# Performance work log

Hardware: AMD Instinct MI355X
Metric: run time of the kernel (lower is better)

## Reference

```python
import jax, jax.numpy as jnp
import numpy as np
from jax import lax

B, S, V, E, H, T = 128, 512, 30000, 256, 256, 9
PAD_ID = 0


def setup_inputs() -> dict:
    key = jax.random.key(0)
    ks = jax.random.split(key, 16)
    u = lambda k, sh, s: jax.random.uniform(k, sh, jnp.float32, -s, s)
    sc = 1.0 / float(np.sqrt(H))
    so = 1.0 / float(np.sqrt(2 * H))
    input_ids = jax.random.randint(ks[0], (B, S), 1, V)
    lengths = jax.random.randint(ks[1], (B,), 1, S + 1)
    mask = jnp.arange(S)[None, :] < lengths[:, None]  # left-contiguous valid mask
    embed_table = jax.random.normal(ks[2], (V, E), jnp.float32).at[PAD_ID].set(0.0)
    return dict(
        input_ids=input_ids,
        mask=mask,
        embed_table=embed_table,
        W_ih_f=u(ks[3], (4 * H, E), sc), W_hh_f=u(ks[4], (4 * H, H), sc), b_f=u(ks[5], (4 * H,), sc),
        W_ih_b=u(ks[6], (4 * H, E), sc), W_hh_b=u(ks[7], (4 * H, H), sc), b_b=u(ks[8], (4 * H,), sc),
        W_out=u(ks[9], (T, 2 * H), so), b_out=u(ks[10], (T,), so),
        start_trans=u(ks[11], (T,), 0.1), end_trans=u(ks[12], (T,), 0.1), trans=u(ks[13], (T, T), 0.1),
    )


def _lstm_dir(xg, W_hh, reverse):
    # xg: [S, B, 4H] precomputed input projection + bias; torch gate order i,f,g,o
    def step(carry, g_in):
        h, c = carry
        g = g_in + h @ W_hh.T
        i, f, gg, o = jnp.split(g, 4, axis=-1)
        c = jax.nn.sigmoid(f) * c + jax.nn.sigmoid(i) * jnp.tanh(gg)
        h = jax.nn.sigmoid(o) * jnp.tanh(c)
        return (h, c), h
    b, hdim = xg.shape[1], W_hh.shape[1]
    init = (jnp.zeros((b, hdim), xg.dtype), jnp.zeros((b, hdim), xg.dtype))
    _, hs = lax.scan(step, init, xg, reverse=reverse)
    return hs  # [S, B, H]


def _emissions(input_ids, embed_table, W_ih_f, W_hh_f, b_f, W_ih_b, W_hh_b, b_b, W_out, b_out):
    x = embed_table[input_ids]                                  # [B, S, E]
    xg_f = jnp.einsum('bse,ge->sbg', x, W_ih_f) + b_f           # [S, B, 4H]
    xg_b = jnp.einsum('bse,ge->sbg', x, W_ih_b) + b_b
    h_f = _lstm_dir(xg_f, W_hh_f, reverse=False)
    h_b = _lstm_dir(xg_b, W_hh_b, reverse=True)
    h = jnp.concatenate([h_f, h_b], axis=-1)                    # [S, B, 2H]
    return jnp.einsum('sbh,th->sbt', h, W_out) + b_out          # [S, B, T]


def reference(input_ids, mask, embed_table, W_ih_f, W_hh_f, b_f, W_ih_b, W_hh_b, b_b,
              W_out, b_out, start_trans, end_trans, trans):
    em = _emissions(input_ids, embed_table, W_ih_f, W_hh_f, b_f, W_ih_b, W_hh_b, b_b, W_out, b_out)
    maskT = mask.T  # [S, B]

    # ---- Viterbi forward (torchcrf._viterbi_decode semantics) ----
    score0 = start_trans + em[0]  # [B, T]

    def vstep(score, inp):
        em_t, m_t = inp  # [B,T], [B]
        nxt = score[:, :, None] + trans[None, :, :] + em_t[:, None, :]  # [B, T, T]
        idx = jnp.argmax(nxt, axis=1)        # [B, T] backpointers
        best = jnp.max(nxt, axis=1)          # [B, T]
        score = jnp.where(m_t[:, None], best, score)
        return score, idx

    score, history = lax.scan(vstep, score0, (em[1:], maskT[1:]))  # history: [S-1, B, T]
    last_tag = jnp.argmax(score + end_trans, axis=-1)              # [B]

    # ---- Backtrace (mask-aware; frontier stays put on padded steps) ----
    def btstep(tag, inp):
        hist_t, m_t = inp  # [B,T], [B]
        out = tag
        prev = jnp.take_along_axis(hist_t, tag[:, None], axis=1)[:, 0]
        tag = jnp.where(m_t, prev, tag)
        return tag, out

    tag0, tags_rest = lax.scan(btstep, last_tag, (history, maskT[1:]), reverse=True)
    tags = jnp.concatenate([tag0[None, :], tags_rest], axis=0).T  # [B, S]
    return jnp.where(mask, tags, 0).astype(jnp.int32)
```

## Files before the change

### kernel.cpp

```cpp
#include <hip/hip_runtime.h>
#include <hip/hip_bf16.h>

#define SEQ   512
#define BATCH 128
#define VOCAB 30000
#define EDIM  256
#define HDIM  256
#define NT    9

__global__ void k_detect(const unsigned char* __restrict__ m, int* __restrict__ flag) {
    __shared__ int ok_sh;
    if (threadIdx.x == 0) ok_sh = 1;
    __syncthreads();
    int b = threadIdx.x;
    const uint4* row = (const uint4*)(m + b * SEQ);
    int ok = 1, prev = 1;
    for (int i = 0; i < SEQ / 16; ++i) {
        uint4 v = row[i];
        unsigned w[4] = {v.x, v.y, v.z, v.w};
        #pragma unroll
        for (int wi = 0; wi < 4; ++wi) {
            #pragma unroll
            for (int j = 0; j < 4; ++j) {
                int byte = (w[wi] >> (8 * j)) & 255;
                if (byte > 1 || byte > prev) ok = 0;
                prev = byte;
            }
        }
    }
    if (!ok) atomicAnd(&ok_sh, 0);
    __syncthreads();
    if (threadIdx.x == 0) *flag = ok_sh;
}

__global__ __launch_bounds__(256) void k_table_gemm(
    const float* __restrict__ emb, const float* __restrict__ Wf,
    const float* __restrict__ Wb, const float* __restrict__ bf,
    const float* __restrict__ bb, float* __restrict__ table) {
    __shared__ __align__(16) float As[64][68];
    __shared__ __align__(16) float Bs[64][68];
    int t  = threadIdx.x;
    int tx = t & 15, ty = t >> 4;
    int n0 = blockIdx.x * 64;
    int v0 = blockIdx.y * 64;
    float acc[4][4] = {};
    for (int kc = 0; kc < 4; ++kc) {
        #pragma unroll
        for (int rr = 0; rr < 4; ++rr) {
            int slot = t + rr * 256;
            int m  = (slot & 15) | ((slot >> 8) << 4);
            int kq = (slot >> 4) & 15;
            int v = v0 + m;
            float4 a = (v < VOCAB)
                ? *(const float4*)&emb[v * EDIM + kc * 64 + kq * 4]
                : make_float4(0.f, 0.f, 0.f, 0.f);
            As[kq * 4 + 0][m] = a.x; As[kq * 4 + 1][m] = a.y;
            As[kq * 4 + 2][m] = a.z; As[kq * 4 + 3][m] = a.w;
            int n = n0 + m;
            const float* Wrow = (n < 1024) ? &Wf[n * 256] : &Wb[(n - 1024) * 256];
            float4 bvec = *(const float4*)&Wrow[kc * 64 + kq * 4];
            Bs[kq * 4 + 0][m] = bvec.x; Bs[kq * 4 + 1][m] = bvec.y;
            Bs[kq * 4 + 2][m] = bvec.z; Bs[kq * 4 + 3][m] = bvec.w;
        }
        __syncthreads();
        #pragma unroll
        for (int k = 0; k < 64; ++k) {
            float4 a = *(const float4*)&As[k][ty * 4];
            float4 b = *(const float4*)&Bs[k][tx * 4];
            acc[0][0] += a.x * b.x; acc[0][1] += a.x * b.y; acc[0][2] += a.x * b.z; acc[0][3] += a.x * b.w;
            acc[1][0] += a.y * b.x; acc[1][1] += a.y * b.y; acc[1][2] += a.y * b.z; acc[1][3] += a.y * b.w;
            acc[2][0] += a.z * b.x; acc[2][1] += a.z * b.y; acc[2][2] += a.z * b.z; acc[2][3] += a.z * b.w;
            acc[3][0] += a.w * b.x; acc[3][1] += a.w * b.y; acc[3][2] += a.w * b.z; acc[3][3] += a.w * b.w;
        }
        __syncthreads();
    }
    int n = n0 + tx * 4;
    const float* bi = (n < 1024) ? &bf[n] : &bb[n - 1024];
    float4 bias = *(const float4*)bi;
    #pragma unroll
    for (int i = 0; i < 4; ++i) {
        int v = v0 + ty * 4 + i;
        if (v < VOCAB) {
            float4 o;
            o.x = acc[i][0] + bias.x; o.y = acc[i][1] + bias.y;
            o.z = acc[i][2] + bias.z; o.w = acc[i][3] + bias.w;
            *(float4*)&table[(size_t)v * 2048 + n] = o;
        }
    }
}

#define DPPXOR(dst, src, CTRL) { \
    int _i = __float_as_int(src); \
    int _r = __builtin_amdgcn_update_dpp(_i, _i, (CTRL), 0xF, 0xF, false); \
    dst = __int_as_float(_r); }

__global__ __attribute__((amdgpu_flat_work_group_size(512, 512), amdgpu_waves_per_eu(4, 4)))
void k_lstm_cl(
    const int* __restrict__ ids, const float* __restrict__ Whhf,
    const float* __restrict__ Whhb, const float* __restrict__ table,
    const float* __restrict__ Wout, float* __restrict__ emp,
    float* hx, int* tagbuf) {
    __shared__ float h_cur[4][256];
    __shared__ float h_em[256];
    __shared__ float sh_g[4][132];
    __shared__ float wout_s[NT][257];
    __shared__ int   sh_ctr;

    const int t   = threadIdx.x;
    const int bid = blockIdx.x;
    const int cluster = bid >> 3;
    const int myd = bid & 7;
    const int dir = cluster & 1;
    const int quad = cluster >> 1;
    const int gbatch = quad * 4 + myd;

    const int lane = t & 63;
    const int wv   = t >> 6;
    const int g    = t >> 4;
    const int kc   = t & 15;

    const int nb = (t >> 5) & 3;
    const int nd = t & 31;

    const int em = t - 256;
    const int etg = em >> 4, el = em & 15;

    const float* Whh = dir ? Whhb : Whhf;

    if (t == 0) sh_ctr = 0;
    for (int idx = t; idx < NT * 256; idx += 512)
        wout_s[idx >> 8][idx & 255] = Wout[(idx >> 8) * 512 + dir * 256 + (idx & 255)];
    for (int idx = t; idx < 1024; idx += 512)
        h_cur[idx >> 8][idx & 255] = 0.f;
    float c_state = 0.f;

    float4 w0_0, w0_1, w0_2, w0_3, w1_0, w1_1, w1_2, w1_3;
    float4 w2_0, w2_1, w2_2, w2_3, w3_0, w3_1, w3_2, w3_3;
    {
        int lr0 = 4 * g, lr1 = 4 * g + 1, lr2 = 4 * g + 2, lr3 = 4 * g + 3;
        int gr0 = (lr0 >> 5) * 256 + myd * 32 + (lr0 & 31);
        int gr1 = (lr1 >> 5) * 256 + myd * 32 + (lr1 & 31);
        int gr2 = (lr2 >> 5) * 256 + myd * 32 + (lr2 & 31);
        int gr3 = (lr3 >> 5) * 256 + myd * 32 + (lr3 & 31);
        const float4* wp0 = (const float4*)(Whh + (size_t)gr0 * 256);
        const float4* wp1 = (const float4*)(Whh + (size_t)gr1 * 256);
        const float4* wp2 = (const float4*)(Whh + (size_t)gr2 * 256);
        const float4* wp3 = (const float4*)(Whh + (size_t)gr3 * 256);
        w0_0 = wp0[kc]; w0_1 = wp0[kc + 16]; w0_2 = wp0[kc + 32]; w0_3 = wp0[kc + 48];
        w1_0 = wp1[kc]; w1_1 = wp1[kc + 16]; w1_2 = wp1[kc + 32]; w1_3 = wp1[kc + 48];
        w2_0 = wp2[kc]; w2_1 = wp2[kc + 16]; w2_2 = wp2[kc + 32]; w2_3 = wp2[kc + 48];
        w3_0 = wp3[kc]; w3_1 = wp3[kc + 16]; w3_2 = wp3[kc + 32]; w3_3 = wp3[kc + 48];
    }
    __syncthreads();

    float xi = 0.f, xf = 0.f, xq = 0.f, xo = 0.f;
    if (t < 128) {
        int s0 = dir ? SEQ - 1 : 0;
        int id = ids[(quad * 4 + nb) * SEQ + s0];
        const float* tb = table + (size_t)id * 2048 + dir * 1024;
        int base = myd * 32 + nd;
        xi = tb[base]; xf = tb[256 + base]; xq = tb[512 + base]; xo = tb[768 + base];
    }

    #pragma unroll 1
    for (int it = 0; it < SEQ; ++it) {
        if (myd < 4 && t < 256) h_em[t] = h_cur[myd][t];

        float a[16];
        #pragma unroll
        for (int m = 0; m < 16; ++m) a[m] = 0.f;

        #define DOTJ(J, W0, W1, W2, W3) { \
            const int off = 4 * (kc + 16 * (J)); \
            _Pragma("unroll") \
            for (int b = 0; b < 4; ++b) { \
                float4 hv = *(const float4*)(&h_cur[b][0] + off); \
                a[b]      += W0.x*hv.x + W0.y*hv.y + W0.z*hv.z + W0.w*hv.w; \
                a[4 + b]  += W1.x*hv.x + W1.y*hv.y + W1.z*hv.z + W1.w*hv.w; \
                a[8 + b]  += W2.x*hv.x + W2.y*hv.y + W2.z*hv.z + W2.w*hv.w; \
                a[12 + b] += W3.x*hv.x + W3.y*hv.y + W3.z*hv.z + W3.w*hv.w; } }
        DOTJ(0, w0_0, w1_0, w2_0, w3_0)
        DOTJ(1, w0_1, w1_1, w2_1, w3_1)
        DOTJ(2, w0_2, w1_2, w2_2, w3_2)
        DOTJ(3, w0_3, w1_3, w2_3, w3_3)
        #undef DOTJ

        #pragma unroll
        for (int m = 0; m < 8; ++m) {
            int bit = kc & 1;
            float sent = bit ? a[m] : a[m + 8];
            float recv; DPPXOR(recv, sent, 0xB1)
            a[m] = (bit ? a[m + 8] : a[m]) + recv;
        }
        #pragma unroll
        for (int m = 0; m < 4; ++m) {
            int bit = kc & 2;
            float sent = bit ? a[m] : a[m + 4];
            float recv; DPPXOR(recv, sent, 0x4E)
            a[m] = (bit ? a[m + 4] : a[m]) + recv;
        }
        #pragma unroll
        for (int m = 0; m < 2; ++m) {
            int bit = kc & 4;
            float sent = bit ? a[m] : a[m + 2];
            float recv = __shfl_xor(sent, 4);
            a[m] = (bit ? a[m + 2] : a[m]) + recv;
        }
        {
            int bit = kc & 8;
            float sent = bit ? a[0] : a[1];
            float recv; DPPXOR(recv, sent, 0x128)
            a[0] = (bit ? a[1] : a[0]) + recv;
        }
        {
            int tile = ((kc & 1) << 3) | ((kc & 2) << 1) | ((kc & 4) >> 1) | ((kc & 8) >> 3);
            sh_g[tile & 3][4 * g + (tile >> 2)] = a[0];
        }
        __syncthreads();

        const int p = it & 1;
        float* hxp = hx + (size_t)p * 65536 + (size_t)cluster * 1024;
        int* tags = tagbuf + p * 512 + cluster * 8;

        if (t < 128) {
            float iv = sh_g[nb][nd]      + xi;
            float fv = sh_g[nb][32 + nd] + xf;
            float gv = sh_g[nb][64 + nd] + xq;
            float ov = sh_g[nb][96 + nd] + xo;
            float si = 1.f / (1.f + expf(-iv));
            float sf = 1.f / (1.f + expf(-fv));
            float so = 1.f / (1.f + expf(-ov));
            float tg = tanhf(gv);
            c_state = sf * c_state + si * tg;
            float hh = so * tanhf(c_state);
            int dl = myd * 32 + nd;
            h_cur[nb][dl] = hh;
            __hip_atomic_store(&hxp[nb * 256 + dl], hh,
                               __ATOMIC_RELAXED, __HIP_MEMORY_SCOPE_AGENT);
            asm volatile("s_waitcnt vmcnt(0)" ::: "memory");
            if (lane == 0) atomicAdd(&sh_ctr, 1);
            if (t == 0) {
                while (__hip_atomic_load(&sh_ctr, __ATOMIC_RELAXED,
                                         __HIP_MEMORY_SCOPE_WORKGROUP) < 2 * (it + 1)) {}
                __hip_atomic_store(&tags[myd], it,
                                   __ATOMIC_RELAXED, __HIP_MEMORY_SCOPE_AGENT);
            }
            if (it < SEQ - 1) {
                int sn = dir ? (SEQ - 2 - it) : (it + 1);
                int id = ids[(quad * 4 + nb) * SEQ + sn];
                const float* tb = table + (size_t)id * 2048 + dir * 1024;
                int base = myd * 32 + nd;
                xi = tb[base]; xf = tb[256 + base]; xq = tb[512 + base]; xo = tb[768 + base];
            }
        } else if (em >= 0 && em < 144 && myd < 4) {
            if (it > 0) {
                int sp = dir ? (SEQ - it) : (it - 1);
                float pe = 0.f;
                #pragma unroll
                for (int j = 0; j < 16; ++j)
                    pe += wout_s[etg][el + 16 * j] * h_em[el + 16 * j];
                pe += __shfl_xor(pe, 1); pe += __shfl_xor(pe, 2);
                pe += __shfl_xor(pe, 4); pe += __shfl_xor(pe, 8);
                if (el == 0)
                    emp[(((size_t)(dir * BATCH) + gbatch) * SEQ + sp) * NT + etg] = pe;
            }
        }

        if (wv != myd) {
            while (__hip_atomic_load(&tags[wv], __ATOMIC_RELAXED,
                                     __HIP_MEMORY_SCOPE_AGENT) != it)
                __builtin_amdgcn_s_sleep(1);
            #pragma unroll
            for (int rep = 0; rep < 2; ++rep) {
                int idx = rep * 64 + lane;
                int b2 = idx >> 5, nd2 = idx & 31;
                float vv = __hip_atomic_load(&hxp[b2 * 256 + wv * 32 + nd2],
                                             __ATOMIC_RELAXED, __HIP_MEMORY_SCOPE_AGENT);
                h_cur[b2][wv * 32 + nd2] = vv;
            }
        }
        __syncthreads();
    }

    if (myd < 4 && t < 256) h_em[t] = h_cur[myd][t];
    __syncthreads();
    if (myd < 4 && t < 144) {
        int etg2 = t >> 4, el2 = t & 15;
        int sp = dir ? 0 : (SEQ - 1);
        float pe = 0.f;
        #pragma unroll
        for (int j = 0; j < 16; ++j)
            pe += wout_s[etg2][el2 + 16 * j] * h_em[el2 + 16 * j];
        pe += __shfl_xor(pe, 1); pe += __shfl_xor(pe, 2);
        pe += __shfl_xor(pe, 4); pe += __shfl_xor(pe, 8);
        if (el2 == 0)
            emp[(((size_t)(dir * BATCH) + gbatch) * SEQ + sp) * NT + etg2] = pe;
    }
}

__global__ __launch_bounds__(64) void k_viterbi(
    const float* __restrict__ emp, const float* __restrict__ b_out,
    const float* __restrict__ start_t, const float* __restrict__ end_t,
    const float* __restrict__ trans, const void* __restrict__ maskp,
    const int* __restrict__ mask_is_bool, int* __restrict__ out) {
    __shared__ float sh_em[SEQ][NT];
    __shared__ float sh_score[NT];
    __shared__ float sh_trans[NT * NT];
    __shared__ unsigned char sh_mask[SEQ];
    __shared__ unsigned char sh_hist[SEQ - 1][NT];
    __shared__ unsigned char sh_tags[SEQ];
    int b = blockIdx.x;
    int t = threadIdx.x;
    int isb = *mask_is_bool;
    for (int idx = t; idx < SEQ * NT; idx += 64) {
        int s = idx / NT, tg = idx % NT;
        sh_em[s][tg] = emp[((size_t)b * SEQ + s) * NT + tg]
                     + emp[(((size_t)BATCH + b) * SEQ + s) * NT + tg]
                     + b_out[tg];
    }
    if (isb) {
        const unsigned char* m8 = (const unsigned char*)maskp;
        for (int idx = t; idx < SEQ; idx += 64) sh_mask[idx] = m8[b * SEQ + idx];
    } else {
        const int* m32 = (const int*)maskp;
        for (int idx = t; idx < SEQ; idx += 64) sh_mask[idx] = (unsigned char)(m32[b * SEQ + idx] != 0);
    }
    for (int idx = t; idx < NT * NT; idx += 64) sh_trans[idx] = trans[idx];
    __syncthreads();
    float sc = 0.f;
    if (t < NT) { sc = start_t[t] + sh_em[0][t]; sh_score[t] = sc; }
    __syncthreads();
    for (int s = 1; s < SEQ; ++s) {
        if (t < NT) {
            float m = -3.4e38f; int bp = 0;
            #pragma unroll
            for (int i = 0; i < NT; ++i) {
                float v = sh_score[i] + sh_trans[i * NT + t];
                if (v > m) { m = v; bp = i; }
            }
            sh_hist[s - 1][t] = (unsigned char)bp;
            float best = m + sh_em[s][t];
            if (sh_mask[s]) sc = best;
        }
        __syncthreads();
        if (t < NT) sh_score[t] = sc;
        __syncthreads();
    }
    if (t == 0) {
        float bb = -3.4e38f; int tag = 0;
        for (int j = 0; j < NT; ++j) {
            float v = sh_score[j] + end_t[j];
            if (v > bb) { bb = v; tag = j; }
        }
        for (int pos = SEQ - 1; pos >= 1; --pos) {
            sh_tags[pos] = (unsigned char)tag;
            if (sh_mask[pos]) tag = sh_hist[pos - 1][tag];
        }
        sh_tags[0] = (unsigned char)tag;
    }
    __syncthreads();
    for (int idx = t; idx < SEQ; idx += 64) {
        out[b * SEQ + idx] = sh_mask[idx] ? (int)sh_tags[idx] : 0;
    }
}

extern "C" void kernel_launch(void* const* d_in, const int* in_sizes, int n_in,
                              void* d_out, int out_size, void* d_ws, size_t ws_size,
                              hipStream_t stream) {
    const int*   ids  = (const int*)d_in[0];
    const void*  mask = d_in[1];
    const float* emb  = (const float*)d_in[2];
    const float* Wihf = (const float*)d_in[3];
    const float* Whhf = (const float*)d_in[4];
    const float* bfv  = (const float*)d_in[5];
    const float* Wihb = (const float*)d_in[6];
    const float* Whhb = (const float*)d_in[7];
    const float* bbv  = (const float*)d_in[8];
    const float* Wout = (const float*)d_in[9];
    const float* bout = (const float*)d_in[10];
    const float* st   = (const float*)d_in[11];
    const float* en   = (const float*)d_in[12];
    const float* tr   = (const float*)d_in[13];
    int* out = (int*)d_out;

    char* ws = (char*)d_ws;
    float* table = (float*)ws;
    float* emp   = (float*)(ws + 245760000);
    float* hx    = (float*)(ws + 245760000 + 4718592);
    int*   tags  = (int*)(ws + 245760000 + 4718592 + 524288);
    int*   flag  = (int*)(ws + 245760000 + 4718592 + 524288 + 4096);

    k_detect<<<1, 128, 0, stream>>>((const unsigned char*)mask, flag);
    dim3 g1(32, 469);
    k_table_gemm<<<g1, 256, 0, stream>>>(emb, Wihf, Wihb, bfv, bbv, table);
    k_lstm_cl<<<512, 512, 0, stream>>>(ids, Whhf, Whhb, table, Wout, emp, hx, tags);
    k_viterbi<<<128, 64, 0, stream>>>(emp, bout, st, en, tr, mask, flag, out);
}
```

Baseline: 3.373 ms.

## Replace per-block shared counter with per-wave ready flags; move emission projection to idle wave

```diff
diff --git a/kernel.cpp b/kernel.cpp
--- a/kernel.cpp
+++ b/kernel.cpp
@@ -104,7 +104,6 @@
     __shared__ float h_em[256];
     __shared__ float sh_g[4][132];
     __shared__ float wout_s[NT][257];
-    __shared__ int   sh_ctr;
 
     const int t   = threadIdx.x;
     const int bid = blockIdx.x;
@@ -122,12 +121,8 @@
     const int nb = (t >> 5) & 3;
     const int nd = t & 31;
 
-    const int em = t - 256;
-    const int etg = em >> 4, el = em & 15;
-
     const float* Whh = dir ? Whhb : Whhf;
 
-    if (t == 0) sh_ctr = 0;
     for (int idx = t; idx < NT * 256; idx += 512)
         wout_s[idx >> 8][idx & 255] = Wout[(idx >> 8) * 512 + dir * 256 + (idx & 255)];
     for (int idx = t; idx < 1024; idx += 512)
@@ -220,7 +215,7 @@
 
         const int p = it & 1;
         float* hxp = hx + (size_t)p * 65536 + (size_t)cluster * 1024;
-        int* tags = tagbuf + p * 512 + cluster * 8;
+        int* tags = tagbuf + p * 1024 + cluster * 16;
 
         if (t < 128) {
             float iv = sh_g[nb][nd]      + xi;
@@ -238,13 +233,9 @@
             __hip_atomic_store(&hxp[nb * 256 + dl], hh,
                                __ATOMIC_RELAXED, __HIP_MEMORY_SCOPE_AGENT);
             asm volatile("s_waitcnt vmcnt(0)" ::: "memory");
-            if (lane == 0) atomicAdd(&sh_ctr, 1);
-            if (t == 0) {
-                while (__hip_atomic_load(&sh_ctr, __ATOMIC_RELAXED,
-                                         __HIP_MEMORY_SCOPE_WORKGROUP) < 2 * (it + 1)) {}
-                __hip_atomic_store(&tags[myd], it,
+            if (lane == 0)
+                __hip_atomic_store(&tags[myd * 2 + wv], it,
                                    __ATOMIC_RELAXED, __HIP_MEMORY_SCOPE_AGENT);
-            }
             if (it < SEQ - 1) {
                 int sn = dir ? (SEQ - 2 - it) : (it + 1);
                 int id = ids[(quad * 4 + nb) * SEQ + sn];
@@ -252,22 +243,12 @@
                 int base = myd * 32 + nd;
                 xi = tb[base]; xf = tb[256 + base]; xq = tb[512 + base]; xo = tb[768 + base];
             }
-        } else if (em >= 0 && em < 144 && myd < 4) {
-            if (it > 0) {
-                int sp = dir ? (SEQ - it) : (it - 1);
-                float pe = 0.f;
-                #pragma unroll
-                for (int j = 0; j < 16; ++j)
-                    pe += wout_s[etg][el + 16 * j] * h_em[el + 16 * j];
-                pe += __shfl_xor(pe, 1); pe += __shfl_xor(pe, 2);
-                pe += __shfl_xor(pe, 4); pe += __shfl_xor(pe, 8);
-                if (el == 0)
-                    emp[(((size_t)(dir * BATCH) + gbatch) * SEQ + sp) * NT + etg] = pe;
-            }
         }
 
         if (wv != myd) {
-            while (__hip_atomic_load(&tags[wv], __ATOMIC_RELAXED,
+            while (__hip_atomic_load(&tags[wv * 2 + 0], __ATOMIC_RELAXED,
+                                     __HIP_MEMORY_SCOPE_AGENT) != it ||
+                   __hip_atomic_load(&tags[wv * 2 + 1], __ATOMIC_RELAXED,
                                      __HIP_MEMORY_SCOPE_AGENT) != it)
                 __builtin_amdgcn_s_sleep(1);
             #pragma unroll
@@ -277,6 +258,31 @@
                 float vv = __hip_atomic_load(&hxp[b2 * 256 + wv * 32 + nd2],
                                              __ATOMIC_RELAXED, __HIP_MEMORY_SCOPE_AGENT);
                 h_cur[b2][wv * 32 + nd2] = vv;
+            }
+        } else if (myd < 4 && it > 0) {
+            int sp = dir ? (SEQ - it) : (it - 1);
+            int eg = lane >> 3, ee = lane & 7;
+            float pe = 0.f;
+            #pragma unroll
+            for (int j = 0; j < 8; ++j) {
+                float4 h4 = *(const float4*)(&h_em[ee * 32 + j * 4]);
+                float4 w4 = *(const float4*)(&wout_s[eg][ee * 32 + j * 4]);
+                pe += h4.x*w4.x + h4.y*w4.y + h4.z*w4.z + h4.w*w4.w;
+            }
+            pe += __shfl_xor(pe, 1); pe += __shfl_xor(pe, 2); pe += __shfl_xor(pe, 4);
+            if (ee == 0)
+                emp[(((size_t)(dir * BATCH) + gbatch) * SEQ + sp) * NT + eg] = pe;
+            if (eg == 0) {
+                float p8 = 0.f;
+                #pragma unroll
+                for (int j = 0; j < 8; ++j) {
+                    float4 h4 = *(const float4*)(&h_em[ee * 32 + j * 4]);
+                    float4 w4 = *(const float4*)(&wout_s[8][ee * 32 + j * 4]);
+                    p8 += h4.x*w4.x + h4.y*w4.y + h4.z*w4.z + h4.w*w4.w;
+                }
+                p8 += __shfl_xor(p8, 1); p8 += __shfl_xor(p8, 2); p8 += __shfl_xor(p8, 4);
+                if (ee == 0)
+                    emp[(((size_t)(dir * BATCH) + gbatch) * SEQ + sp) * NT + 8] = p8;
             }
         }
         __syncthreads();
@@ -388,7 +394,7 @@
     float* emp   = (float*)(ws + 245760000);
     float* hx    = (float*)(ws + 245760000 + 4718592);
     int*   tags  = (int*)(ws + 245760000 + 4718592 + 524288);
-    int*   flag  = (int*)(ws + 245760000 + 4718592 + 524288 + 4096);
+    int*   flag  = (int*)(ws + 245760000 + 4718592 + 524288 + 8192);
 
     k_detect<<<1, 128, 0, stream>>>((const unsigned char*)mask, flag);
     dim3 g1(32, 469);
```

New measurement: 3.723 ms. 10.4% more time.
